# Kernel optimization log

Measured on AMD Instinct MI355X. Metric: run time of the kernel, lower is better.

## Reference

```python
import jax, jax.numpy as jnp
import numpy as np

OBS = 128; N_AGENT = 16; N_ACTION = 8; N_LAYER = 2; HID = 128
GE = 256; LE = 256; F1 = 512; F2 = 512


def _edges(batch_size, n):
    # all ordered pairs (i, j), i != j, within each sample; GCNConv adds self-loops
    i, j = np.meshgrid(np.arange(n), np.arange(n), indexing='ij')
    m = i != j
    src0, dst0 = i[m], j[m]                      # [n*(n-1)]
    off = (np.arange(batch_size) * n)[:, None]
    src = (src0[None, :] + off).reshape(-1)
    dst = (dst0[None, :] + off).reshape(-1)
    return jnp.asarray(src, jnp.int32), jnp.asarray(dst, jnp.int32)


def setup_inputs() -> dict:
    key = jax.random.key(0)
    ks = jax.random.split(key, 16)
    g = lambda k, shp, fan: jax.random.normal(k, shp, jnp.float32) / np.sqrt(fan)
    return {
        'obs_j': jax.random.normal(ks[0], (2048, N_AGENT, OBS), jnp.float32),
        'W_pre': g(ks[1], (OBS, HID), OBS), 'b_pre': jnp.zeros((HID,), jnp.float32),
        'W_gcn': g(ks[2], (N_LAYER, HID, HID), HID), 'b_gcn': jnp.zeros((N_LAYER, HID), jnp.float32),
        'W_post': g(ks[3], (HID, GE), HID), 'b_post': jnp.zeros((GE,), jnp.float32),
        'W_loc': g(ks[4], (OBS, LE), OBS), 'b_loc': jnp.zeros((LE,), jnp.float32),
        'W1': g(ks[5], (GE + LE, F1), GE + LE), 'b1': jnp.zeros((F1,), jnp.float32),
        'W2': g(ks[6], (F1, F2), F1), 'b2': jnp.zeros((F2,), jnp.float32),
        'W3': g(ks[7], (F2, N_ACTION), F2), 'b3': jnp.zeros((N_ACTION,), jnp.float32),
    }


def reference(obs_j, W_pre, b_pre, W_gcn, b_gcn, W_post, b_post,
              W_loc, b_loc, W1, b1, W2, b2, W3, b3):
    B, n, _ = obs_j.shape
    N = B * n
    obs = obs_j.reshape(N, OBS)
    x = jax.nn.relu(obs @ W_pre + b_pre)          # [N, HID]

    src, dst = _edges(B, n)
    # GCNConv with self-loops on a fully-connected graph: deg = n for every node,
    # edge norm = 1/sqrt(deg_i*deg_j) = 1/n for every (A+I) edge.
    inv_n = jnp.float32(1.0) / n
    for l in range(N_LAYER):
        h = x @ W_gcn[l]                          # lin (no bias inside propagate)
        agg = jax.ops.segment_sum(h[src], dst, num_segments=N)  # neighbor gather/scatter
        x = jax.nn.relu((agg + h) * inv_n + b_gcn[l])            # + self-loop msg, bias

    g = x.reshape(B, n, HID).mean(axis=1)         # global_mean_pool over each graph
    g = jax.nn.relu(g @ W_post + b_post)          # [B, GE]
    loc = jax.nn.relu(obs @ W_loc + b_loc)        # [B*n, LE]
    gi = jnp.repeat(g, n, axis=0)                 # repeat_interleave over agents
    z = jnp.concatenate([gi, loc], axis=1)
    z = jax.nn.relu(z @ W1 + b1)
    z = jax.nn.relu(z @ W2 + b2)
    q = z @ W3 + b3
    return q.reshape(B, n, N_ACTION)
```

## Files before the change

### kernel.cpp

```cpp
#include <hip/hip_runtime.h>
#include <hip/hip_bf16.h>
#include <stdint.h>

typedef __bf16 bf16;
typedef __bf16 bf16x4 __attribute__((ext_vector_type(4)));
typedef __bf16 bf16x8 __attribute__((ext_vector_type(8)));
typedef float f32x4 __attribute__((ext_vector_type(4)));

#define MFMA(a, b, c) __builtin_amdgcn_mfma_f32_16x16x32_bf16(a, b, c, 0, 0, 0)
#define GL(p) ((const __attribute__((address_space(1))) void*)(p))
#define SH(p) ((__attribute__((address_space(3))) void*)(p))

__device__ inline void tp(const float* W, bf16* WT, int id, int shiftK, int N) {
  int K = 1 << shiftK;
  int n = id >> shiftK;
  int k = id & (K - 1);
  WT[id] = (bf16)W[(size_t)k * N + n];
}

__global__ __launch_bounds__(256) void prep_all(
    const float* __restrict__ W1, const float* __restrict__ W2,
    bf16* __restrict__ W1T, bf16* __restrict__ W2T,
    const float* __restrict__ Wpre, const float* __restrict__ Wloc,
    const float* __restrict__ Wgcn, const float* __restrict__ Wpost,
    bf16* __restrict__ WpreLocT, bf16* __restrict__ Wg0T, bf16* __restrict__ Wg1T,
    bf16* __restrict__ WpostT,
    const float* __restrict__ bpre, const float* __restrict__ bloc,
    float* __restrict__ biasPL, float* __restrict__ outq) {
  __shared__ bf16 tile[64 * 68];
  int blk = blockIdx.x;
  int tid = threadIdx.x;
  if (blk < 128) {
    const float* W = (blk < 64) ? W1 : W2;
    bf16* WT = (blk < 64) ? W1T : W2T;
    int t = blk & 63;
    int tk0 = (t >> 3) * 64, tn0 = (t & 7) * 64;
#pragma unroll
    for (int p = 0; p < 4; p++) {
      int kr = p * 16 + (tid >> 4), nc = (tid & 15) * 4;
      float4 f = *(const float4*)(W + (size_t)(tk0 + kr) * 512 + tn0 + nc);
      bf16x4 v; v[0] = (bf16)f.x; v[1] = (bf16)f.y; v[2] = (bf16)f.z; v[3] = (bf16)f.w;
      *(bf16x4*)&tile[kr * 68 + nc] = v;
    }
    __syncthreads();
#pragma unroll
    for (int p = 0; p < 4; p++) {
      int nr = p * 16 + (tid >> 4), kc = (tid & 15) * 4;
      bf16x4 v;
#pragma unroll
      for (int i = 0; i < 4; i++) v[i] = tile[(kc + i) * 68 + nr];
      *(bf16x4*)(WT + (size_t)(tn0 + nr) * 512 + tk0 + kc) = v;
    }
    return;
  }
  blk -= 128;
  if (blk < 448) {
    int id = blk * 256 + tid;
    if (id < 16384) { tp(Wpre, WpreLocT, id, 7, 128); return; } id -= 16384;
    if (id < 32768) { tp(Wloc, WpreLocT + 16384, id, 7, 256); return; } id -= 32768;
    if (id < 16384) { tp(Wgcn, Wg0T, id, 7, 128); return; } id -= 16384;
    if (id < 16384) { tp(Wgcn + 16384, Wg1T, id, 7, 128); return; } id -= 16384;
    tp(Wpost, WpostT, id, 7, 256);
    return;
  }
  blk -= 448;
  if (blk == 0) {
    if (tid < 128) biasPL[tid] = bpre[tid];
    biasPL[128 + tid] = bloc[tid];
    return;
  }
  blk -= 1;
  float4 z = {0.f, 0.f, 0.f, 0.f};
#pragma unroll
  for (int i = 0; i < 4; i++)
    ((float4*)outq)[(size_t)blk * 1024 + i * 256 + tid] = z;
}

__global__ __launch_bounds__(256, 4) void k1c(
    const float* __restrict__ obs, const bf16* __restrict__ WpreLocT,
    const float* __restrict__ biasPL,
    const bf16* __restrict__ Wg0T, const bf16* __restrict__ Wg1T,
    const bf16* __restrict__ WpostT, const float* __restrict__ b_gcn,
    const float* __restrict__ b_post,
    const bf16* __restrict__ W1T, const float* __restrict__ b1,
    bf16* __restrict__ loc, float* __restrict__ h) {
  __shared__ bf16 smem[16384];
  bf16* As = smem;
  bf16* Bs = smem + 8192;

  const int tid = threadIdx.x;
  const int id = blockIdx.x;
  const int s = id >> 3;
  const int n_idx = s % 3;
  const int m0 = ((id & 7) + 8 * (s / 3)) * 128;
  const int n0 = n_idx * 128;

  f32x4 acc[4][4] = {};
  const int lane = tid & 63, wave = tid >> 6;
  const int wm = (wave >> 1) * 64, wn = (wave & 1) * 64;
  const int lm = lane & 15, quad = lane >> 4;

  for (int k0 = 0; k0 < 128; k0 += 64) {
#pragma unroll
    for (int it = 0; it < 4; it++) {
      int idx = it * 256 + tid;
      int row = idx >> 3;
      int c = idx & 7;
      int cv8 = c ^ (row & 7);
      int kk = k0 + cv8 * 8;
      const float* src = obs + (size_t)(m0 + row) * 128 + kk;
      float4 f0 = *(const float4*)src;
      float4 f1 = *(const float4*)(src + 4);
      bf16x8 v;
      v[0] = (bf16)f0.x; v[1] = (bf16)f0.y; v[2] = (bf16)f0.z; v[3] = (bf16)f0.w;
      v[4] = (bf16)f1.x; v[5] = (bf16)f1.y; v[6] = (bf16)f1.z; v[7] = (bf16)f1.w;
      *(bf16x8*)&As[row * 64 + c * 8] = v;
      const bf16* gb = WpreLocT + (size_t)(n0 + row) * 128 + kk;
      __builtin_amdgcn_global_load_lds(GL(gb), SH(&Bs[(idx & ~63) * 8]), 16, 0, 0);
    }
    __syncthreads();
#pragma unroll
    for (int ks = 0; ks < 2; ks++) {
      const int ua = quad + ks * 4;
      bf16x8 a[4], b[4];
#pragma unroll
      for (int i = 0; i < 4; i++) {
        int r = wm + lm + i * 16;
        a[i] = *(const bf16x8*)&As[r * 64 + ((ua ^ (r & 7)) * 8)];
      }
#pragma unroll
      for (int j = 0; j < 4; j++) {
        int r = wn + lm + j * 16;
        b[j] = *(const bf16x8*)&Bs[r * 64 + ((ua ^ (r & 7)) * 8)];
      }
#pragma unroll
      for (int i = 0; i < 4; i++)
#pragma unroll
        for (int j = 0; j < 4; j++)
          acc[i][j] = MFMA(a[i], b[j], acc[i][j]);
    }
    __syncthreads();
  }

  if (n_idx == 0) {
    bf16* xs = smem;
    bf16* x2 = smem + 2176;
    bf16* gS = smem + 4352;
#pragma unroll
    for (int i = 0; i < 4; i++) {
      int sl = (wave >> 1) * 4 + i;
#pragma unroll
      for (int j = 0; j < 4; j++) {
        int col = wn + j * 16 + lm;
        float bb = biasPL[col];
        float v = 0.f;
#pragma unroll
        for (int r = 0; r < 4; r++) v += fmaxf(acc[i][j][r] + bb, 0.f);
        v += __shfl_xor(v, 16);
        v += __shfl_xor(v, 32);
        if (quad == 0) xs[sl * 136 + col] = (bf16)(v * 0.0625f);
        else if (quad == 1) xs[(8 + sl) * 136 + col] = (bf16)0.f;
      }
    }
    __syncthreads();
    {
      f32x4 c2[2] = {};
#pragma unroll
      for (int ku = 0; ku < 4; ++ku) {
        bf16x8 a = *(const bf16x8*)&xs[lm * 136 + (ku * 4 + quad) * 8];
#pragma unroll
        for (int jn = 0; jn < 2; ++jn) {
          int col = (wave * 2 + jn) * 16 + lm;
          bf16x8 b = *(const bf16x8*)&Wg0T[(size_t)col * 128 + ku * 32 + quad * 8];
          c2[jn] = MFMA(a, b, c2[jn]);
        }
      }
      __syncthreads();
#pragma unroll
      for (int jn = 0; jn < 2; ++jn) {
        int col = (wave * 2 + jn) * 16 + lm;
        float bb = b_gcn[col];
#pragma unroll
        for (int r = 0; r < 4; ++r)
          x2[(quad * 4 + r) * 136 + col] = (bf16)fmaxf(c2[jn][r] + bb, 0.f);
      }
    }
    __syncthreads();
    {
      f32x4 c2[2] = {};
#pragma unroll
      for (int ku = 0; ku < 4; ++ku) {
        bf16x8 a = *(const bf16x8*)&x2[lm * 136 + (ku * 4 + quad) * 8];
#pragma unroll
        for (int jn = 0; jn < 2; ++jn) {
          int col = (wave * 2 + jn) * 16 + lm;
          bf16x8 b = *(const bf16x8*)&Wg1T[(size_t)col * 128 + ku * 32 + quad * 8];
          c2[jn] = MFMA(a, b, c2[jn]);
        }
      }
      __syncthreads();
#pragma unroll
      for (int jn = 0; jn < 2; ++jn) {
        int col = (wave * 2 + jn) * 16 + lm;
        float bb = b_gcn[128 + col];
#pragma unroll
        for (int r = 0; r < 4; ++r)
          xs[(quad * 4 + r) * 136 + col] = (bf16)fmaxf(c2[jn][r] + bb, 0.f);
      }
    }
    __syncthreads();
    {
      f32x4 c3[4] = {};
#pragma unroll
      for (int ku = 0; ku < 4; ++ku) {
        bf16x8 a = *(const bf16x8*)&xs[lm * 136 + (ku * 4 + quad) * 8];
#pragma unroll
        for (int jn = 0; jn < 4; ++jn) {
          int col = (wave * 4 + jn) * 16 + lm;
          bf16x8 b = *(const bf16x8*)&WpostT[(size_t)col * 128 + ku * 32 + quad * 8];
          c3[jn] = MFMA(a, b, c3[jn]);
        }
      }
#pragma unroll
      for (int jn = 0; jn < 4; ++jn) {
        int col = (wave * 4 + jn) * 16 + lm;
        float bb = b_post[col];
#pragma unroll
        for (int r = 0; r < 4; ++r)
          gS[(quad * 4 + r) * 264 + col] = (bf16)fmaxf(c3[jn][r] + bb, 0.f);
      }
    }
    __syncthreads();
    {
      f32x4 hacc[8] = {};
#pragma unroll
      for (int ku = 0; ku < 8; ++ku) {
        bf16x8 a = *(const bf16x8*)&gS[lm * 264 + ku * 32 + quad * 8];
#pragma unroll
        for (int jn = 0; jn < 8; ++jn) {
          int col = (wave * 8 + jn) * 16 + lm;
          bf16x8 b = *(const bf16x8*)&W1T[(size_t)col * 512 + ku * 32 + quad * 8];
          hacc[jn] = MFMA(a, b, hacc[jn]);
        }
      }
      int sample0 = m0 >> 4;
#pragma unroll
      for (int jn = 0; jn < 8; ++jn) {
        int col = (wave * 8 + jn) * 16 + lm;
        float bb = b1[col];
#pragma unroll
        for (int r = 0; r < 4; ++r) {
          int row = quad * 4 + r;
          if (row < 8)
            h[(size_t)(sample0 + row) * 512 + col] = hacc[jn][r] + bb;
        }
      }
    }
  } else {
#pragma unroll
    for (int i = 0; i < 4; i++)
#pragma unroll
      for (int j = 0; j < 4; j++) {
        int col = wn + j * 16 + lm;
        float bb = biasPL[n0 + col];
#pragma unroll
        for (int r = 0; r < 4; r++) {
          int row = wm + i * 16 + quad * 4 + r;
          smem[row * 128 + col] = (bf16)fmaxf(acc[i][j][r] + bb, 0.f);
        }
      }
    __syncthreads();
    const int coff = n0 - 128;
#pragma unroll
    for (int c = 0; c < 8; c++) {
      int ci = c * 256 + tid;
      int row = ci >> 4, col8 = (ci & 15) * 8;
      *(bf16x8*)&loc[(size_t)(m0 + row) * 256 + coff + col8] = *(const bf16x8*)&smem[row * 128 + col8];
    }
  }
}

template <bool HREP>
__global__ __launch_bounds__(256, 4) void gemm_k(
    const bf16* __restrict__ Ab, const bf16* __restrict__ BT,
    const float* __restrict__ bias, const float* __restrict__ hrep,
    bf16* __restrict__ C,
    const float* __restrict__ W3, const float* __restrict__ b3,
    float* __restrict__ outq) {
  __shared__ bf16 smem[16384];
  bf16* As = smem;
  bf16* Bs = smem + 8192;

  const int tid = threadIdx.x;
  const int id = blockIdx.x;
  const int s = id >> 3;
  const int n_idx = s & 3;
  const int m0 = ((id & 7) + 8 * (s >> 2)) * 128;
  const int n0 = n_idx * 128;

  f32x4 acc[4][4] = {};
  const int lane = tid & 63, wave = tid >> 6;
  const int wm = (wave >> 1) * 64, wn = (wave & 1) * 64;
  const int lm = lane & 15, quad = lane >> 4;

  const int KTOT = HREP ? 256 : 512;
  for (int k0 = 0; k0 < KTOT; k0 += 64) {
#pragma unroll
    for (int it = 0; it < 4; it++) {
      int idx = it * 256 + tid;
      int row = idx >> 3;
      int c = idx & 7;
      int cv8 = c ^ (row & 7);
      int kk = k0 + cv8 * 8;
      const bf16* ga = HREP ? (Ab + (size_t)(m0 + row) * 256 + kk)
                            : (Ab + (size_t)(m0 + row) * 512 + kk);
      __builtin_amdgcn_global_load_lds(GL(ga), SH(&As[(idx & ~63) * 8]), 16, 0, 0);
      const bf16* gb = HREP ? (BT + (size_t)(n0 + row) * 512 + 256 + kk)
                            : (BT + (size_t)(n0 + row) * 512 + kk);
      __builtin_amdgcn_global_load_lds(GL(gb), SH(&Bs[(idx & ~63) * 8]), 16, 0, 0);
    }
    __syncthreads();
#pragma unroll
    for (int ks = 0; ks < 2; ks++) {
      const int ua = quad + ks * 4;
      bf16x8 a[4], b[4];
#pragma unroll
      for (int i = 0; i < 4; i++) {
        int r = wm + lm + i * 16;
        a[i] = *(const bf16x8*)&As[r * 64 + ((ua ^ (r & 7)) * 8)];
      }
#pragma unroll
      for (int j = 0; j < 4; j++) {
        int r = wn + lm + j * 16;
        b[j] = *(const bf16x8*)&Bs[r * 64 + ((ua ^ (r & 7)) * 8)];
      }
#pragma unroll
      for (int i = 0; i < 4; i++)
#pragma unroll
        for (int j = 0; j < 4; j++)
          acc[i][j] = MFMA(a[i], b[j], acc[i][j]);
    }
    __syncthreads();
  }

  if (HREP) {
#pragma unroll
    for (int i = 0; i < 4; i++) {
      int sample = (m0 + wm + i * 16) >> 4;
#pragma unroll
      for (int j = 0; j < 4; j++) {
        int col = n0 + wn + j * 16 + lm;
        float hv = hrep[(size_t)sample * 512 + col];
#pragma unroll
        for (int r = 0; r < 4; r++) {
          int row = wm + i * 16 + quad * 4 + r;
          smem[row * 128 + (col - n0)] = (bf16)fmaxf(acc[i][j][r] + hv, 0.f);
        }
      }
    }
    __syncthreads();
#pragma unroll
    for (int c = 0; c < 8; c++) {
      int ci = c * 256 + tid;
      int row = ci >> 4, col8 = (ci & 15) * 8;
      *(bf16x8*)&C[(size_t)(m0 + row) * 512 + n0 + col8] = *(const bf16x8*)&smem[row * 128 + col8];
    }
  } else {
#pragma unroll
    for (int i = 0; i < 4; i++)
#pragma unroll
      for (int j = 0; j < 4; j++) {
        int col = wn + j * 16 + lm;
        float bb = bias[n0 + col];
#pragma unroll
        for (int r = 0; r < 4; r++) {
          int row = wm + i * 16 + quad * 4 + r;
          smem[row * 128 + col] = (bf16)fmaxf(acc[i][j][r] + bb, 0.f);
        }
      }
    __syncthreads();
    int n = lane & 7;
    int kg = lane >> 3;
    float w3r[16];
#pragma unroll
    for (int i = 0; i < 16; i++) w3r[i] = W3[(size_t)(n0 + kg * 16 + i) * 8 + n];
    float bn = (n_idx == 0) ? b3[n] : 0.f;
    int rbase = wave * 32;
    for (int rr = 0; rr < 32; rr++) {
      const bf16* zr = &smem[(rbase + rr) * 128 + kg * 16];
      bf16x8 z0 = *(const bf16x8*)zr;
      bf16x8 z1v = *(const bf16x8*)(zr + 8);
      float v = 0.f;
#pragma unroll
      for (int i = 0; i < 8; i++) v += (float)z0[i] * w3r[i];
#pragma unroll
      for (int i = 0; i < 8; i++) v += (float)z1v[i] * w3r[8 + i];
      v += __shfl_down(v, 32);
      v += __shfl_down(v, 16);
      v += __shfl_down(v, 8);
      if (lane < 8) atomicAdd(&outq[(size_t)(m0 + rbase + rr) * 8 + n], v + bn);
    }
  }
}

extern "C" void kernel_launch(void* const* d_in, const int* in_sizes, int n_in,
                              void* d_out, int out_size, void* d_ws, size_t ws_size,
                              hipStream_t stream) {
  const float* obs    = (const float*)d_in[0];
  const float* W_pre  = (const float*)d_in[1];
  const float* b_pre  = (const float*)d_in[2];
  const float* W_gcn  = (const float*)d_in[3];
  const float* b_gcn  = (const float*)d_in[4];
  const float* W_post = (const float*)d_in[5];
  const float* b_post = (const float*)d_in[6];
  const float* W_loc  = (const float*)d_in[7];
  const float* b_loc  = (const float*)d_in[8];
  const float* W1     = (const float*)d_in[9];
  const float* b1     = (const float*)d_in[10];
  const float* W2     = (const float*)d_in[11];
  const float* b2     = (const float*)d_in[12];
  const float* W3     = (const float*)d_in[13];
  const float* b3     = (const float*)d_in[14];
  float* out = (float*)d_out;

  char* p = (char*)d_ws;
  auto alloc = [&](size_t bytes) { char* r = p; p += (bytes + 255) & ~(size_t)255; return r; };
  bf16* WpreLocT = (bf16*)alloc(384 * 128 * 2);
  float* biasPL  = (float*)alloc(384 * 4);
  bf16* Wg0T   = (bf16*)alloc(128 * 128 * 2);
  bf16* Wg1T   = (bf16*)alloc(128 * 128 * 2);
  bf16* WpostT = (bf16*)alloc(256 * 128 * 2);
  bf16* W1T    = (bf16*)alloc(512 * 512 * 2);
  bf16* W2T    = (bf16*)alloc(512 * 512 * 2);
  bf16* locB   = (bf16*)alloc((size_t)32768 * 256 * 2);
  float* hB    = (float*)alloc((size_t)2048 * 512 * 4);
  bf16* z1B    = (bf16*)alloc((size_t)32768 * 512 * 2);

  prep_all<<<641, 256, 0, stream>>>(W1, W2, W1T, W2T,
                                    W_pre, W_loc, W_gcn, W_post,
                                    WpreLocT, Wg0T, Wg1T, WpostT,
                                    b_pre, b_loc, biasPL, out);
  k1c<<<768, 256, 0, stream>>>(obs, WpreLocT, biasPL,
                               Wg0T, Wg1T, WpostT, b_gcn, b_post,
                               W1T, b1, locB, hB);
  gemm_k<true><<<1024, 256, 0, stream>>>(locB, W1T, nullptr, hB, z1B,
                                         nullptr, nullptr, nullptr);
  gemm_k<false><<<1024, 256, 0, stream>>>(z1B, W2T, b2, nullptr, nullptr,
                                          W3, b3, out);
}
```

Baseline: 172.0 us.

## Fuse three GEMM stages into one kernel with per-row-tile spin barriers

Merges the encoder/GCN kernel and the two MLP GEMM kernels into a single 1024-block launch. The four blocks that share a 128-row tile synchronise through global atomic counters between stages, so later stages wait only on their own row tile rather than on a whole-grid kernel boundary. This removes two launch gaps and the tail idle between them. In exchange it depends on all four cooperating blocks being resident at once (1024 blocks at 4 per CU fits on 256 CUs), adds atomic spin overhead, and needs the flags zeroed in prep.

```diff
diff --git a/kernel.cpp b/kernel.cpp
--- a/kernel.cpp
+++ b/kernel.cpp
@@ -26,7 +26,7 @@
     bf16* __restrict__ WpreLocT, bf16* __restrict__ Wg0T, bf16* __restrict__ Wg1T,
     bf16* __restrict__ WpostT,
     const float* __restrict__ bpre, const float* __restrict__ bloc,
-    float* __restrict__ biasPL, float* __restrict__ outq) {
+    float* __restrict__ biasPL, float* __restrict__ outq, int* __restrict__ flags) {
   __shared__ bf16 tile[64 * 68];
   int blk = blockIdx.x;
   int tid = threadIdx.x;
@@ -67,6 +67,8 @@
   if (blk == 0) {
     if (tid < 128) biasPL[tid] = bpre[tid];
     biasPL[128 + tid] = bloc[tid];
+    flags[tid] = 0;
+    flags[256 + tid] = 0;
     return;
   }
   blk -= 1;
@@ -76,217 +78,29 @@
     ((float4*)outq)[(size_t)blk * 1024 + i * 256 + tid] = z;
 }
 
-__global__ __launch_bounds__(256, 4) void k1c(
+__device__ inline void gbar(int* flag) {
+  __syncthreads();
+  if (threadIdx.x == 0) {
+    __threadfence();
+    atomicAdd(flag, 1);
+    while (__hip_atomic_load(flag, __ATOMIC_RELAXED, __HIP_MEMORY_SCOPE_AGENT) < 4)
+      __builtin_amdgcn_s_sleep(8);
+  }
+  __syncthreads();
+  __threadfence();
+}
+
+__global__ __launch_bounds__(256, 4) void fused(
     const float* __restrict__ obs, const bf16* __restrict__ WpreLocT,
     const float* __restrict__ biasPL,
     const bf16* __restrict__ Wg0T, const bf16* __restrict__ Wg1T,
     const bf16* __restrict__ WpostT, const float* __restrict__ b_gcn,
     const float* __restrict__ b_post,
     const bf16* __restrict__ W1T, const float* __restrict__ b1,
-    bf16* __restrict__ loc, float* __restrict__ h) {
-  __shared__ bf16 smem[16384];
-  bf16* As = smem;
-  bf16* Bs = smem + 8192;
-
-  const int tid = threadIdx.x;
-  const int id = blockIdx.x;
-  const int s = id >> 3;
-  const int n_idx = s % 3;
-  const int m0 = ((id & 7) + 8 * (s / 3)) * 128;
-  const int n0 = n_idx * 128;
-
-  f32x4 acc[4][4] = {};
-  const int lane = tid & 63, wave = tid >> 6;
-  const int wm = (wave >> 1) * 64, wn = (wave & 1) * 64;
-  const int lm = lane & 15, quad = lane >> 4;
-
-  for (int k0 = 0; k0 < 128; k0 += 64) {
-#pragma unroll
-    for (int it = 0; it < 4; it++) {
-      int idx = it * 256 + tid;
-      int row = idx >> 3;
-      int c = idx & 7;
-      int cv8 = c ^ (row & 7);
-      int kk = k0 + cv8 * 8;
-      const float* src = obs + (size_t)(m0 + row) * 128 + kk;
-      float4 f0 = *(const float4*)src;
-      float4 f1 = *(const float4*)(src + 4);
-      bf16x8 v;
-      v[0] = (bf16)f0.x; v[1] = (bf16)f0.y; v[2] = (bf16)f0.z; v[3] = (bf16)f0.w;
-      v[4] = (bf16)f1.x; v[5] = (bf16)f1.y; v[6] = (bf16)f1.z; v[7] = (bf16)f1.w;
-      *(bf16x8*)&As[row * 64 + c * 8] = v;
-      const bf16* gb = WpreLocT + (size_t)(n0 + row) * 128 + kk;
-      __builtin_amdgcn_global_load_lds(GL(gb), SH(&Bs[(idx & ~63) * 8]), 16, 0, 0);
-    }
-    __syncthreads();
-#pragma unroll
-    for (int ks = 0; ks < 2; ks++) {
-      const int ua = quad + ks * 4;
-      bf16x8 a[4], b[4];
-#pragma unroll
-      for (int i = 0; i < 4; i++) {
-        int r = wm + lm + i * 16;
-        a[i] = *(const bf16x8*)&As[r * 64 + ((ua ^ (r & 7)) * 8)];
-      }
-#pragma unroll
-      for (int j = 0; j < 4; j++) {
-        int r = wn + lm + j * 16;
-        b[j] = *(const bf16x8*)&Bs[r * 64 + ((ua ^ (r & 7)) * 8)];
-      }
-#pragma unroll
-      for (int i = 0; i < 4; i++)
-#pragma unroll
-        for (int j = 0; j < 4; j++)
-          acc[i][j] = MFMA(a[i], b[j], acc[i][j]);
-    }
-    __syncthreads();
-  }
-
-  if (n_idx == 0) {
-    bf16* xs = smem;
-    bf16* x2 = smem + 2176;
-    bf16* gS = smem + 4352;
-#pragma unroll
-    for (int i = 0; i < 4; i++) {
-      int sl = (wave >> 1) * 4 + i;
-#pragma unroll
-      for (int j = 0; j < 4; j++) {
-        int col = wn + j * 16 + lm;
-        float bb = biasPL[col];
-        float v = 0.f;
-#pragma unroll
-        for (int r = 0; r < 4; r++) v += fmaxf(acc[i][j][r] + bb, 0.f);
-        v += __shfl_xor(v, 16);
-        v += __shfl_xor(v, 32);
-        if (quad == 0) xs[sl * 136 + col] = (bf16)(v * 0.0625f);
-        else if (quad == 1) xs[(8 + sl) * 136 + col] = (bf16)0.f;
-      }
-    }
-    __syncthreads();
-    {
-      f32x4 c2[2] = {};
-#pragma unroll
-      for (int ku = 0; ku < 4; ++ku) {
-        bf16x8 a = *(const bf16x8*)&xs[lm * 136 + (ku * 4 + quad) * 8];
-#pragma unroll
-        for (int jn = 0; jn < 2; ++jn) {
-          int col = (wave * 2 + jn) * 16 + lm;
-          bf16x8 b = *(const bf16x8*)&Wg0T[(size_t)col * 128 + ku * 32 + quad * 8];
-          c2[jn] = MFMA(a, b, c2[jn]);
-        }
-      }
-      __syncthreads();
-#pragma unroll
-      for (int jn = 0; jn < 2; ++jn) {
-        int col = (wave * 2 + jn) * 16 + lm;
-        float bb = b_gcn[col];
-#pragma unroll
-        for (int r = 0; r < 4; ++r)
-          x2[(quad * 4 + r) * 136 + col] = (bf16)fmaxf(c2[jn][r] + bb, 0.f);
-      }
-    }
-    __syncthreads();
-    {
-      f32x4 c2[2] = {};
-#pragma unroll
-      for (int ku = 0; ku < 4; ++ku) {
-        bf16x8 a = *(const bf16x8*)&x2[lm * 136 + (ku * 4 + quad) * 8];
-#pragma unroll
-        for (int jn = 0; jn < 2; ++jn) {
-          int col = (wave * 2 + jn) * 16 + lm;
-          bf16x8 b = *(const bf16x8*)&Wg1T[(size_t)col * 128 + ku * 32 + quad * 8];
-          c2[jn] = MFMA(a, b, c2[jn]);
-        }
-      }
-      __syncthreads();
-#pragma unroll
-      for (int jn = 0; jn < 2; ++jn) {
-        int col = (wave * 2 + jn) * 16 + lm;
-        float bb = b_gcn[128 + col];
-#pragma unroll
-        for (int r = 0; r < 4; ++r)
-          xs[(quad * 4 + r) * 136 + col] = (bf16)fmaxf(c2[jn][r] + bb, 0.f);
-      }
-    }
-    __syncthreads();
-    {
-      f32x4 c3[4] = {};
-#pragma unroll
-      for (int ku = 0; ku < 4; ++ku) {
-        bf16x8 a = *(const bf16x8*)&xs[lm * 136 + (ku * 4 + quad) * 8];
-#pragma unroll
-        for (int jn = 0; jn < 4; ++jn) {
-          int col = (wave * 4 + jn) * 16 + lm;
-          bf16x8 b = *(const bf16x8*)&WpostT[(size_t)col * 128 + ku * 32 + quad * 8];
-          c3[jn] = MFMA(a, b, c3[jn]);
-        }
-      }
-#pragma unroll
-      for (int jn = 0; jn < 4; ++jn) {
-        int col = (wave * 4 + jn) * 16 + lm;
-        float bb = b_post[col];
-#pragma unroll
-        for (int r = 0; r < 4; ++r)
-          gS[(quad * 4 + r) * 264 + col] = (bf16)fmaxf(c3[jn][r] + bb, 0.f);
-      }
-    }
-    __syncthreads();
-    {
-      f32x4 hacc[8] = {};
-#pragma unroll
-      for (int ku = 0; ku < 8; ++ku) {
-        bf16x8 a = *(const bf16x8*)&gS[lm * 264 + ku * 32 + quad * 8];
-#pragma unroll
-        for (int jn = 0; jn < 8; ++jn) {
-          int col = (wave * 8 + jn) * 16 + lm;
-          bf16x8 b = *(const bf16x8*)&W1T[(size_t)col * 512 + ku * 32 + quad * 8];
-          hacc[jn] = MFMA(a, b, hacc[jn]);
-        }
-      }
-      int sample0 = m0 >> 4;
-#pragma unroll
-      for (int jn = 0; jn < 8; ++jn) {
-        int col = (wave * 8 + jn) * 16 + lm;
-        float bb = b1[col];
-#pragma unroll
-        for (int r = 0; r < 4; ++r) {
-          int row = quad * 4 + r;
-          if (row < 8)
-            h[(size_t)(sample0 + row) * 512 + col] = hacc[jn][r] + bb;
-        }
-      }
-    }
-  } else {
-#pragma unroll
-    for (int i = 0; i < 4; i++)
-#pragma unroll
-      for (int j = 0; j < 4; j++) {
-        int col = wn + j * 16 + lm;
-        float bb = biasPL[n0 + col];
-#pragma unroll
-        for (int r = 0; r < 4; r++) {
-          int row = wm + i * 16 + quad * 4 + r;
-          smem[row * 128 + col] = (bf16)fmaxf(acc[i][j][r] + bb, 0.f);
-        }
-      }
-    __syncthreads();
-    const int coff = n0 - 128;
-#pragma unroll
-    for (int c = 0; c < 8; c++) {
-      int ci = c * 256 + tid;
-      int row = ci >> 4, col8 = (ci & 15) * 8;
-      *(bf16x8*)&loc[(size_t)(m0 + row) * 256 + coff + col8] = *(const bf16x8*)&smem[row * 128 + col8];
-    }
-  }
-}
-
-template <bool HREP>
-__global__ __launch_bounds__(256, 4) void gemm_k(
-    const bf16* __restrict__ Ab, const bf16* __restrict__ BT,
-    const float* __restrict__ bias, const float* __restrict__ hrep,
-    bf16* __restrict__ C,
+    const bf16* __restrict__ W2T, const float* __restrict__ b2,
     const float* __restrict__ W3, const float* __restrict__ b3,
-    float* __restrict__ outq) {
+    bf16* __restrict__ loc, float* __restrict__ h, bf16* __restrict__ z1,
+    float* __restrict__ outq, int* __restrict__ flags) {
   __shared__ bf16 smem[16384];
   bf16* As = smem;
   bf16* Bs = smem + 8192;
@@ -295,62 +109,242 @@
   const int id = blockIdx.x;
   const int s = id >> 3;
   const int n_idx = s & 3;
-  const int m0 = ((id & 7) + 8 * (s >> 2)) * 128;
+  const int mt = (id & 7) + 8 * (s >> 2);
+  const int m0 = mt * 128;
   const int n0 = n_idx * 128;
 
-  f32x4 acc[4][4] = {};
   const int lane = tid & 63, wave = tid >> 6;
   const int wm = (wave >> 1) * 64, wn = (wave & 1) * 64;
   const int lm = lane & 15, quad = lane >> 4;
 
-  const int KTOT = HREP ? 256 : 512;
-  for (int k0 = 0; k0 < KTOT; k0 += 64) {
-#pragma unroll
-    for (int it = 0; it < 4; it++) {
-      int idx = it * 256 + tid;
-      int row = idx >> 3;
-      int c = idx & 7;
-      int cv8 = c ^ (row & 7);
-      int kk = k0 + cv8 * 8;
-      const bf16* ga = HREP ? (Ab + (size_t)(m0 + row) * 256 + kk)
-                            : (Ab + (size_t)(m0 + row) * 512 + kk);
-      __builtin_amdgcn_global_load_lds(GL(ga), SH(&As[(idx & ~63) * 8]), 16, 0, 0);
-      const bf16* gb = HREP ? (BT + (size_t)(n0 + row) * 512 + 256 + kk)
-                            : (BT + (size_t)(n0 + row) * 512 + kk);
-      __builtin_amdgcn_global_load_lds(GL(gb), SH(&Bs[(idx & ~63) * 8]), 16, 0, 0);
-    }
-    __syncthreads();
-#pragma unroll
-    for (int ks = 0; ks < 2; ks++) {
-      const int ua = quad + ks * 4;
-      bf16x8 a[4], b[4];
+  if (n_idx < 3) {
+    f32x4 acc[4][4] = {};
+    for (int k0 = 0; k0 < 128; k0 += 64) {
+#pragma unroll
+      for (int it = 0; it < 4; it++) {
+        int idx = it * 256 + tid;
+        int row = idx >> 3;
+        int c = idx & 7;
+        int cv8 = c ^ (row & 7);
+        int kk = k0 + cv8 * 8;
+        const float* src = obs + (size_t)(m0 + row) * 128 + kk;
+        float4 f0 = *(const float4*)src;
+        float4 f1 = *(const float4*)(src + 4);
+        bf16x8 v;
+        v[0] = (bf16)f0.x; v[1] = (bf16)f0.y; v[2] = (bf16)f0.z; v[3] = (bf16)f0.w;
+        v[4] = (bf16)f1.x; v[5] = (bf16)f1.y; v[6] = (bf16)f1.z; v[7] = (bf16)f1.w;
+        *(bf16x8*)&As[row * 64 + c * 8] = v;
+        const bf16* gb = WpreLocT + (size_t)(n0 + row) * 128 + kk;
+        __builtin_amdgcn_global_load_lds(GL(gb), SH(&Bs[(idx & ~63) * 8]), 16, 0, 0);
+      }
+      __syncthreads();
+#pragma unroll
+      for (int ks = 0; ks < 2; ks++) {
+        const int ua = quad + ks * 4;
+        bf16x8 a[4], b[4];
+#pragma unroll
+        for (int i = 0; i < 4; i++) {
+          int r = wm + lm + i * 16;
+          a[i] = *(const bf16x8*)&As[r * 64 + ((ua ^ (r & 7)) * 8)];
+        }
+#pragma unroll
+        for (int j = 0; j < 4; j++) {
+          int r = wn + lm + j * 16;
+          b[j] = *(const bf16x8*)&Bs[r * 64 + ((ua ^ (r & 7)) * 8)];
+        }
+#pragma unroll
+        for (int i = 0; i < 4; i++)
+#pragma unroll
+          for (int j = 0; j < 4; j++)
+            acc[i][j] = MFMA(a[i], b[j], acc[i][j]);
+      }
+      __syncthreads();
+    }
+
+    if (n_idx == 0) {
+      bf16* xs = smem;
+      bf16* x2 = smem + 2176;
+      bf16* gS = smem + 4352;
 #pragma unroll
       for (int i = 0; i < 4; i++) {
-        int r = wm + lm + i * 16;
-        a[i] = *(const bf16x8*)&As[r * 64 + ((ua ^ (r & 7)) * 8)];
-      }
-#pragma unroll
-      for (int j = 0; j < 4; j++) {
-        int r = wn + lm + j * 16;
-        b[j] = *(const bf16x8*)&Bs[r * 64 + ((ua ^ (r & 7)) * 8)];
-      }
+        int sl = (wave >> 1) * 4 + i;
+#pragma unroll
+        for (int j = 0; j < 4; j++) {
+          int col = wn + j * 16 + lm;
+          float bb = biasPL[col];
+          float v = 0.f;
+#pragma unroll
+          for (int r = 0; r < 4; r++) v += fmaxf(acc[i][j][r] + bb, 0.f);
+          v += __shfl_xor(v, 16);
+          v += __shfl_xor(v, 32);
+          if (quad == 0) xs[sl * 136 + col] = (bf16)(v * 0.0625f);
+          else if (quad == 1) xs[(8 + sl) * 136 + col] = (bf16)0.f;
+        }
+      }
+      __syncthreads();
+      {
+        f32x4 c2[2] = {};
+#pragma unroll
+        for (int ku = 0; ku < 4; ++ku) {
+          bf16x8 a = *(const bf16x8*)&xs[lm * 136 + (ku * 4 + quad) * 8];
+#pragma unroll
+          for (int jn = 0; jn < 2; ++jn) {
+            int col = (wave * 2 + jn) * 16 + lm;
+            bf16x8 b = *(const bf16x8*)&Wg0T[(size_t)col * 128 + ku * 32 + quad * 8];
+            c2[jn] = MFMA(a, b, c2[jn]);
+          }
+        }
+        __syncthreads();
+#pragma unroll
+        for (int jn = 0; jn < 2; ++jn) {
+          int col = (wave * 2 + jn) * 16 + lm;
+          float bb = b_gcn[col];
+#pragma unroll
+          for (int r = 0; r < 4; ++r)
+            x2[(quad * 4 + r) * 136 + col] = (bf16)fmaxf(c2[jn][r] + bb, 0.f);
+        }
+      }
+      __syncthreads();
+      {
+        f32x4 c2[2] = {};
+#pragma unroll
+        for (int ku = 0; ku < 4; ++ku) {
+          bf16x8 a = *(const bf16x8*)&x2[lm * 136 + (ku * 4 + quad) * 8];
+#pragma unroll
+          for (int jn = 0; jn < 2; ++jn) {
+            int col = (wave * 2 + jn) * 16 + lm;
+            bf16x8 b = *(const bf16x8*)&Wg1T[(size_t)col * 128 + ku * 32 + quad * 8];
+            c2[jn] = MFMA(a, b, c2[jn]);
+          }
+        }
+        __syncthreads();
+#pragma unroll
+        for (int jn = 0; jn < 2; ++jn) {
+          int col = (wave * 2 + jn) * 16 + lm;
+          float bb = b_gcn[128 + col];
+#pragma unroll
+          for (int r = 0; r < 4; ++r)
+            xs[(quad * 4 + r) * 136 + col] = (bf16)fmaxf(c2[jn][r] + bb, 0.f);
+        }
+      }
+      __syncthreads();
+      {
+        f32x4 c3[4] = {};
+#pragma unroll
+        for (int ku = 0; ku < 4; ++ku) {
+          bf16x8 a = *(const bf16x8*)&xs[lm * 136 + (ku * 4 + quad) * 8];
+#pragma unroll
+          for (int jn = 0; jn < 4; ++jn) {
+            int col = (wave * 4 + jn) * 16 + lm;
+            bf16x8 b = *(const bf16x8*)&WpostT[(size_t)col * 128 + ku * 32 + quad * 8];
+            c3[jn] = MFMA(a, b, c3[jn]);
+          }
+        }
+#pragma unroll
+        for (int jn = 0; jn < 4; ++jn) {
+          int col = (wave * 4 + jn) * 16 + lm;
+          float bb = b_post[col];
+#pragma unroll
+          for (int r = 0; r < 4; ++r)
+            gS[(quad * 4 + r) * 264 + col] = (bf16)fmaxf(c3[jn][r] + bb, 0.f);
+        }
+      }
+      __syncthreads();
+      {
+        f32x4 hacc[8] = {};
+#pragma unroll
+        for (int ku = 0; ku < 8; ++ku) {
+          bf16x8 a = *(const bf16x8*)&gS[lm * 264 + ku * 32 + quad * 8];
+#pragma unroll
+          for (int jn = 0; jn < 8; ++jn) {
+            int col = (wave * 8 + jn) * 16 + lm;
+            bf16x8 b = *(const bf16x8*)&W1T[(size_t)col * 512 + ku * 32 + quad * 8];
+            hacc[jn] = MFMA(a, b, hacc[jn]);
+          }
+        }
+        int sample0 = m0 >> 4;
+#pragma unroll
+        for (int jn = 0; jn < 8; ++jn) {
+          int col = (wave * 8 + jn) * 16 + lm;
+          float bb = b1[col];
+#pragma unroll
+          for (int r = 0; r < 4; ++r) {
+            int row = quad * 4 + r;
+            if (row < 8)
+              h[(size_t)(sample0 + row) * 512 + col] = hacc[jn][r] + bb;
+          }
+        }
+      }
+    } else {
 #pragma unroll
       for (int i = 0; i < 4; i++)
 #pragma unroll
-        for (int j = 0; j < 4; j++)
-          acc[i][j] = MFMA(a[i], b[j], acc[i][j]);
-    }
-    __syncthreads();
-  }
-
-  if (HREP) {
+        for (int j = 0; j < 4; j++) {
+          int col = wn + j * 16 + lm;
+          float bb = biasPL[n0 + col];
+#pragma unroll
+          for (int r = 0; r < 4; r++) {
+            int row = wm + i * 16 + quad * 4 + r;
+            smem[row * 128 + col] = (bf16)fmaxf(acc[i][j][r] + bb, 0.f);
+          }
+        }
+      __syncthreads();
+      const int coff = n0 - 128;
+#pragma unroll
+      for (int c = 0; c < 8; c++) {
+        int ci = c * 256 + tid;
+        int row = ci >> 4, col8 = (ci & 15) * 8;
+        *(bf16x8*)&loc[(size_t)(m0 + row) * 256 + coff + col8] = *(const bf16x8*)&smem[row * 128 + col8];
+      }
+    }
+  }
+  gbar(&flags[mt]);
+
+  {
+    f32x4 acc[4][4] = {};
+    for (int k0 = 0; k0 < 256; k0 += 64) {
+#pragma unroll
+      for (int it = 0; it < 4; it++) {
+        int idx = it * 256 + tid;
+        int row = idx >> 3;
+        int c = idx & 7;
+        int cv8 = c ^ (row & 7);
+        int kk = k0 + cv8 * 8;
+        const bf16* ga = loc + (size_t)(m0 + row) * 256 + kk;
+        __builtin_amdgcn_global_load_lds(GL(ga), SH(&As[(idx & ~63) * 8]), 16, 0, 0);
+        const bf16* gb = W1T + (size_t)(n0 + row) * 512 + 256 + kk;
+        __builtin_amdgcn_global_load_lds(GL(gb), SH(&Bs[(idx & ~63) * 8]), 16, 0, 0);
+      }
+      __syncthreads();
+#pragma unroll
+      for (int ks = 0; ks < 2; ks++) {
+        const int ua = quad + ks * 4;
+        bf16x8 a[4], b[4];
+#pragma unroll
+        for (int i = 0; i < 4; i++) {
+          int r = wm + lm + i * 16;
+          a[i] = *(const bf16x8*)&As[r * 64 + ((ua ^ (r & 7)) * 8)];
+        }
+#pragma unroll
+        for (int j = 0; j < 4; j++) {
+          int r = wn + lm + j * 16;
+          b[j] = *(const bf16x8*)&Bs[r * 64 + ((ua ^ (r & 7)) * 8)];
+        }
+#pragma unroll
+        for (int i = 0; i < 4; i++)
+#pragma unroll
+          for (int j = 0; j < 4; j++)
+            acc[i][j] = MFMA(a[i], b[j], acc[i][j]);
+      }
+      __syncthreads();
+    }
 #pragma unroll
     for (int i = 0; i < 4; i++) {
       int sample = (m0 + wm + i * 16) >> 4;
 #pragma unroll
       for (int j = 0; j < 4; j++) {
         int col = n0 + wn + j * 16 + lm;
-        float hv = hrep[(size_t)sample * 512 + col];
+        float hv = h[(size_t)sample * 512 + col];
 #pragma unroll
         for (int r = 0; r < 4; r++) {
           int row = wm + i * 16 + quad * 4 + r;
@@ -363,15 +357,55 @@
     for (int c = 0; c < 8; c++) {
       int ci = c * 256 + tid;
       int row = ci >> 4, col8 = (ci & 15) * 8;
-      *(bf16x8*)&C[(size_t)(m0 + row) * 512 + n0 + col8] = *(const bf16x8*)&smem[row * 128 + col8];
-    }
-  } else {
+      *(bf16x8*)&z1[(size_t)(m0 + row) * 512 + n0 + col8] = *(const bf16x8*)&smem[row * 128 + col8];
+    }
+  }
+  gbar(&flags[256 + mt]);
+
+  {
+    f32x4 acc[4][4] = {};
+    for (int k0 = 0; k0 < 512; k0 += 64) {
+#pragma unroll
+      for (int it = 0; it < 4; it++) {
+        int idx = it * 256 + tid;
+        int row = idx >> 3;
+        int c = idx & 7;
+        int cv8 = c ^ (row & 7);
+        int kk = k0 + cv8 * 8;
+        const bf16* ga = z1 + (size_t)(m0 + row) * 512 + kk;
+        __builtin_amdgcn_global_load_lds(GL(ga), SH(&As[(idx & ~63) * 8]), 16, 0, 0);
+        const bf16* gb = W2T + (size_t)(n0 + row) * 512 + kk;
+        __builtin_amdgcn_global_load_lds(GL(gb), SH(&Bs[(idx & ~63) * 8]), 16, 0, 0);
+      }
+      __syncthreads();
+#pragma unroll
+      for (int ks = 0; ks < 2; ks++) {
+        const int ua = quad + ks * 4;
+        bf16x8 a[4], b[4];
+#pragma unroll
+        for (int i = 0; i < 4; i++) {
+          int r = wm + lm + i * 16;
+          a[i] = *(const bf16x8*)&As[r * 64 + ((ua ^ (r & 7)) * 8)];
+        }
+#pragma unroll
+        for (int j = 0; j < 4; j++) {
+          int r = wn + lm + j * 16;
+          b[j] = *(const bf16x8*)&Bs[r * 64 + ((ua ^ (r & 7)) * 8)];
+        }
+#pragma unroll
+        for (int i = 0; i < 4; i++)
+#pragma unroll
+          for (int j = 0; j < 4; j++)
+            acc[i][j] = MFMA(a[i], b[j], acc[i][j]);
+      }
+      __syncthreads();
+    }
 #pragma unroll
     for (int i = 0; i < 4; i++)
 #pragma unroll
       for (int j = 0; j < 4; j++) {
         int col = wn + j * 16 + lm;
-        float bb = bias[n0 + col];
+        float bb = b2[n0 + col];
 #pragma unroll
         for (int r = 0; r < 4; r++) {
           int row = wm + i * 16 + quad * 4 + r;
@@ -435,16 +469,14 @@
   bf16* locB   = (bf16*)alloc((size_t)32768 * 256 * 2);
   float* hB    = (float*)alloc((size_t)2048 * 512 * 4);
   bf16* z1B    = (bf16*)alloc((size_t)32768 * 512 * 2);
+  int* flags   = (int*)alloc(512 * 4);
 
   prep_all<<<641, 256, 0, stream>>>(W1, W2, W1T, W2T,
                                     W_pre, W_loc, W_gcn, W_post,
                                     WpreLocT, Wg0T, Wg1T, WpostT,
-                                    b_pre, b_loc, biasPL, out);
-  k1c<<<768, 256, 0, stream>>>(obs, WpreLocT, biasPL,
-                               Wg0T, Wg1T, WpostT, b_gcn, b_post,
-                               W1T, b1, locB, hB);
-  gemm_k<true><<<1024, 256, 0, stream>>>(locB, W1T, nullptr, hB, z1B,
-                                         nullptr, nullptr, nullptr);
-  gemm_k<false><<<1024, 256, 0, stream>>>(z1B, W2T, b2, nullptr, nullptr,
-                                          W3, b3, out);
+                                    b_pre, b_loc, biasPL, out, flags);
+  fused<<<1024, 256, 0, stream>>>(obs, WpreLocT, biasPL,
+                                  Wg0T, Wg1T, WpostT, b_gcn, b_post,
+                                  W1T, b1, W2T, b2, W3, b3,
+                                  locB, hB, z1B, out, flags);
 }
```

Result: slower. 501.9 us (+191.8%).

## Double-buffer LDS tiles in gemm_k with K-step 32 prefetch

Applied to the files above, without the earlier changes.

Splits the shared memory into two buffers of 32-wide K tiles and issues the global-to-LDS loads for the next tile before computing the current one. This lets memory loads overlap MFMA work and drops one barrier per iteration. The cost is twice as many loop iterations with smaller tiles and a new XOR swizzle for the 32-column layout. The total shared memory footprint stays the same.

```diff
diff --git a/kernel.cpp b/kernel.cpp
--- a/kernel.cpp
+++ b/kernel.cpp
@@ -288,8 +288,6 @@
     const float* __restrict__ W3, const float* __restrict__ b3,
     float* __restrict__ outq) {
   __shared__ bf16 smem[16384];
-  bf16* As = smem;
-  bf16* Bs = smem + 8192;
 
   const int tid = threadIdx.x;
   const int id = blockIdx.x;
@@ -303,43 +301,54 @@
   const int wm = (wave >> 1) * 64, wn = (wave & 1) * 64;
   const int lm = lane & 15, quad = lane >> 4;
 
-  const int KTOT = HREP ? 256 : 512;
-  for (int k0 = 0; k0 < KTOT; k0 += 64) {
-#pragma unroll
-    for (int it = 0; it < 4; it++) {
+  auto stage = [&](int kt, int buf) {
+    bf16* Ad = smem + buf * 8192;
+    bf16* Bd = smem + buf * 8192 + 4096;
+    int k0 = kt * 32;
+#pragma unroll
+    for (int it = 0; it < 2; it++) {
       int idx = it * 256 + tid;
-      int row = idx >> 3;
-      int c = idx & 7;
-      int cv8 = c ^ (row & 7);
-      int kk = k0 + cv8 * 8;
+      int row = idx >> 2;
+      int c = idx & 3;
+      int cv = c ^ ((row >> 1) & 3);
+      int kk = k0 + cv * 8;
       const bf16* ga = HREP ? (Ab + (size_t)(m0 + row) * 256 + kk)
                             : (Ab + (size_t)(m0 + row) * 512 + kk);
-      __builtin_amdgcn_global_load_lds(GL(ga), SH(&As[(idx & ~63) * 8]), 16, 0, 0);
+      __builtin_amdgcn_global_load_lds(GL(ga), SH(&Ad[(idx & ~63) * 8]), 16, 0, 0);
       const bf16* gb = HREP ? (BT + (size_t)(n0 + row) * 512 + 256 + kk)
                             : (BT + (size_t)(n0 + row) * 512 + kk);
-      __builtin_amdgcn_global_load_lds(GL(gb), SH(&Bs[(idx & ~63) * 8]), 16, 0, 0);
-    }
-    __syncthreads();
-#pragma unroll
-    for (int ks = 0; ks < 2; ks++) {
-      const int ua = quad + ks * 4;
-      bf16x8 a[4], b[4];
-#pragma unroll
-      for (int i = 0; i < 4; i++) {
-        int r = wm + lm + i * 16;
-        a[i] = *(const bf16x8*)&As[r * 64 + ((ua ^ (r & 7)) * 8)];
-      }
-#pragma unroll
-      for (int j = 0; j < 4; j++) {
-        int r = wn + lm + j * 16;
-        b[j] = *(const bf16x8*)&Bs[r * 64 + ((ua ^ (r & 7)) * 8)];
-      }
-#pragma unroll
-      for (int i = 0; i < 4; i++)
-#pragma unroll
-        for (int j = 0; j < 4; j++)
-          acc[i][j] = MFMA(a[i], b[j], acc[i][j]);
-    }
+      __builtin_amdgcn_global_load_lds(GL(gb), SH(&Bd[(idx & ~63) * 8]), 16, 0, 0);
+    }
+  };
+
+  auto compute = [&](int buf) {
+    const bf16* Ar = smem + buf * 8192;
+    const bf16* Br = smem + buf * 8192 + 4096;
+    bf16x8 a[4], b[4];
+#pragma unroll
+    for (int i = 0; i < 4; i++) {
+      int r = wm + lm + i * 16;
+      a[i] = *(const bf16x8*)&Ar[r * 32 + ((quad ^ ((r >> 1) & 3)) * 8)];
+    }
+#pragma unroll
+    for (int j = 0; j < 4; j++) {
+      int r = wn + lm + j * 16;
+      b[j] = *(const bf16x8*)&Br[r * 32 + ((quad ^ ((r >> 1) & 3)) * 8)];
+    }
+#pragma unroll
+    for (int i = 0; i < 4; i++)
+#pragma unroll
+      for (int j = 0; j < 4; j++)
+        acc[i][j] = MFMA(a[i], b[j], acc[i][j]);
+  };
+
+  const int NIT = HREP ? 8 : 16;
+  stage(0, 0);
+  __syncthreads();
+#pragma unroll 2
+  for (int i = 0; i < NIT; ++i) {
+    if (i + 1 < NIT) stage(i + 1, (i + 1) & 1);
+    compute(i & 1);
     __syncthreads();
   }
 
```

Result: faster. 163.4 us (-5.0%).
